# Performance work log

Measured on AMD Instinct MI355X. Metric: run time of the kernel, lower is better.

Reference implementation:

```python
import jax, jax.numpy as jnp
import numpy as np

N, F_IN, HID, HEADS, NCLS, E = 50000, 512, 64, 4, 64, 800000
NEG_SLOPE = 0.2
EPS = 1e-16


def setup_inputs() -> dict:
    key = jax.random.key(0)
    ks = jax.random.split(key, 10)
    s = 0.1
    return {
        "x": jax.random.normal(ks[0], (N, F_IN), jnp.float32),
        "edge_index": jax.random.randint(ks[1], (2, E), 0, N, jnp.int64),
        "W1": jax.random.normal(ks[2], (F_IN, HEADS * HID), jnp.float32) * s,
        "a_src1": jax.random.normal(ks[3], (HEADS, HID), jnp.float32) * s,
        "a_dst1": jax.random.normal(ks[4], (HEADS, HID), jnp.float32) * s,
        "b1": jax.random.normal(ks[5], (HEADS * HID,), jnp.float32) * s,
        "W2": jax.random.normal(ks[6], (HEADS * HID, NCLS), jnp.float32) * s,
        "a_src2": jax.random.normal(ks[7], (1, NCLS), jnp.float32) * s,
        "a_dst2": jax.random.normal(ks[8], (1, NCLS), jnp.float32) * s,
        "b2": jax.random.normal(ks[9], (NCLS,), jnp.float32) * s,
    }


def gat_conv(x, W, a_src, a_dst, b, src, dst):
    H, C = a_src.shape
    h = (x @ W).reshape(-1, H, C)                     # [N, H, C]
    # per-node attention halves, gathered per edge -> [E', H]
    al_src = jnp.einsum("nhc,hc->nh", h, a_src)
    al_dst = jnp.einsum("nhc,hc->nh", h, a_dst)
    e = jax.nn.leaky_relu(al_src[src] + al_dst[dst], NEG_SLOPE)
    # segment softmax over destination neighborhoods
    m = jax.ops.segment_max(e, dst, num_segments=x.shape[0])
    ex = jnp.exp(e - m[dst])
    denom = jax.ops.segment_sum(ex, dst, num_segments=x.shape[0])
    alpha = ex / (denom[dst] + EPS)                   # [E', H]
    out = jax.ops.segment_sum(alpha[:, :, None] * h[src], dst,
                              num_segments=x.shape[0])  # [N, H, C]
    return out.reshape(-1, H * C) + b


def reference(x, edge_index, W1, a_src1, a_dst1, b1, W2, a_src2, a_dst2, b2):
    n = x.shape[0]
    loop = jnp.arange(n, dtype=edge_index.dtype)
    src = jnp.concatenate([edge_index[0], loop])       # add self loops (PyG default)
    dst = jnp.concatenate([edge_index[1], loop])
    h = gat_conv(x, W1, a_src1, a_dst1, b1, src, dst)
    h = jax.nn.elu(h)                                  # dropout is identity in eval
    out = gat_conv(h, W2, a_src2, a_dst2, b2, src, dst)
    return jax.nn.log_softmax(out, axis=1)
```

## Files before the change

kernel.cpp:

```cpp
#include <hip/hip_runtime.h>
#include <math.h>

#define F_IN 512
#define HC1 256
#define HEADS 4
#define HID 64
#define NCLS 64
#define NEG_SLOPE 0.2f
#define EPS_DENOM 1e-16f

using short8 = __attribute__((ext_vector_type(8))) short;
using f32x4  = __attribute__((ext_vector_type(4))) float;

__device__ inline float wave_sum(float v) {
#pragma unroll
  for (int s = 32; s > 0; s >>= 1) v += __shfl_xor(v, s);
  return v;
}

__device__ inline unsigned short f2bf(float f) {
  unsigned int u = __float_as_uint(f);
  u = (u + 0x7FFF + ((u >> 16) & 1)) >> 16;
  return (unsigned short)u;
}
__device__ inline float bflo(unsigned int u) { return __uint_as_float(u << 16); }
__device__ inline float bfhi(unsigned int u) { return __uint_as_float(u & 0xFFFF0000u); }

__device__ inline unsigned int cvtpk_bf16(float lo, float hi) {
  unsigned int r;
  asm("v_cvt_pk_bf16_f32 %0, %1, %2" : "=v"(r) : "v"(lo), "v"(hi));
  return r;
}

__device__ inline void async_copy16(const void* g, void* l) {
  __builtin_amdgcn_global_load_lds((const __attribute__((address_space(1))) void*)g,
                                   (__attribute__((address_space(3))) void*)l, 16, 0, 0);
}

__global__ void castT_kernel(const float* __restrict__ W, unsigned short* __restrict__ WT,
                             int K, int Nn) {
  int id = blockIdx.x * blockDim.x + threadIdx.x;
  if (id >= K * Nn) return;
  int n = id / K, k = id % K;
  WT[id] = f2bf(W[(size_t)k * Nn + n]);
}


__global__ void hist_kernel(const int* __restrict__ dst, int E, int* __restrict__ cnt) {
  int i = blockIdx.x * blockDim.x + threadIdx.x;
  int stride = gridDim.x * blockDim.x;
  for (int e = i; e < E; e += stride) atomicAdd(&cnt[dst[e]], 1);
}

__global__ void scan_blocks_kernel(const int* __restrict__ cnt, int n,
                                   int* __restrict__ rowoff, int* __restrict__ cursor,
                                   int* __restrict__ bsum) {
  __shared__ int wpart[16];
  int b = blockIdx.x, tid = threadIdx.x;
  int i = b * 1024 + tid;
  int lane = tid & 63, wid = tid >> 6;
  int v = (i < n) ? (cnt[i] + 1) : 0;
  int x = v;
#pragma unroll
  for (int s = 1; s < 64; s <<= 1) {
    int t = __shfl_up(x, s);
    if (lane >= s) x += t;
  }
  if (lane == 63) wpart[wid] = x;
  __syncthreads();
  if (wid == 0) {
    int p = (lane < 16) ? wpart[lane] : 0;
#pragma unroll
    for (int s = 1; s < 16; s <<= 1) {
      int t = __shfl_up(p, s);
      if (lane >= s) p += t;
    }
    if (lane < 16) wpart[lane] = p;
  }
  __syncthreads();
  int incl = x + (wid ? wpart[wid - 1] : 0);
  if (i < n) { rowoff[i + 1] = incl; cursor[i] = incl - v; }
  if (tid == 1023) bsum[b] = incl;
  if (b == 0 && tid == 0) rowoff[0] = 0;
}

__global__ void scan_partials_kernel(int* __restrict__ bsum, int nb) {
  int lane = threadIdx.x;
  int v = (lane < nb) ? bsum[lane] : 0;
  int x = v;
#pragma unroll
  for (int s = 1; s < 64; s <<= 1) {
    int t = __shfl_up(x, s);
    if (lane >= s) x += t;
  }
  if (lane < nb) bsum[lane] = x - v;
}

__global__ void scan_add_kernel(int n, int* __restrict__ rowoff, int* __restrict__ cursor,
                                const int* __restrict__ bsum) {
  int i = blockIdx.x * 1024 + threadIdx.x;
  int off = bsum[blockIdx.x];
  if (i < n) { rowoff[i + 1] += off; cursor[i] += off; }
}

__global__ void scatter_kernel(const int* __restrict__ src, const int* __restrict__ dst,
                               int E, int n, int* __restrict__ cursor, int* __restrict__ esrc) {
  int i = blockIdx.x * blockDim.x + threadIdx.x;
  int stride = gridDim.x * blockDim.x;
  for (int e = i; e < E + n; e += stride) {
    int s, d;
    if (e < E) { s = src[e]; d = dst[e]; } else { s = e - E; d = s; }
    int pos = atomicAdd(&cursor[d], 1);
    esrc[pos] = s;
  }
}


__global__ __launch_bounds__(256)
void gemm1_fused_kernel(const float* __restrict__ A, const unsigned short* __restrict__ BT,
                        unsigned short* __restrict__ Cb,
                        const float* __restrict__ as1, const float* __restrict__ ad1,
                        float* __restrict__ als, float* __restrict__ ald, int M) {
  constexpr int BM = 64, BN = 256, BK = 32, K = F_IN, Nn = HC1;
  __shared__ float          Af[2][BM * BK];
  __shared__ unsigned short Bh[2][BN * BK];
  const int t = threadIdx.x;
  const int lane = t & 63;
  const int w = t >> 6;
  const int wc = w * 64;
  const int row0 = blockIdx.x * BM;
  const int lrow = lane & 15;
  const int lkf = (lane >> 4) * 8;

  auto stageA = [&](int buf, int k0) {
#pragma unroll
    for (int i = 0; i < 2; ++i) {
      int c = i * 256 + t;
      int r = c >> 3, slot = c & 7;
      int grow = row0 + r; if (grow > M - 1) grow = M - 1;
      const float* g = A + (size_t)grow * K + k0 + ((slot ^ (r & 7)) << 2);
      async_copy16(g, (char*)&Af[buf][0] + (size_t)(i * 256 + w * 64) * 16);
    }
  };
  auto stageB = [&](int buf, int k0) {
#pragma unroll
    for (int i = 0; i < 4; ++i) {
      int c = i * 256 + t;
      int r = c >> 2, slot = c & 3;
      const unsigned short* g = BT + (size_t)r * K + k0 + ((slot ^ (r & 3)) << 3);
      async_copy16(g, (char*)&Bh[buf][0] + (size_t)(i * 256 + w * 64) * 16);
    }
  };

  f32x4 acc[4][4] = {};
  stageA(0, 0); stageB(0, 0);
  int cur = 0;
  for (int k0 = 0; k0 < K; k0 += BK) {
    __syncthreads();
    if (k0 + BK < K) { stageA(cur ^ 1, k0 + BK); stageB(cur ^ 1, k0 + BK); }
    short8 a[4], b[4];
#pragma unroll
    for (int m = 0; m < 4; ++m) {
      int r = m * 16 + lrow;
      int s0 = lkf >> 2;
      const char* base = (const char*)&Af[cur][0] + (size_t)r * 128;
      float4 f0 = *(const float4*)(base + (((s0    ) ^ (r & 7)) << 4));
      float4 f1 = *(const float4*)(base + (((s0 | 1) ^ (r & 7)) << 4));
      union { short8 s; uint4 u; } pk;
      pk.u.x = cvtpk_bf16(f0.x, f0.y); pk.u.y = cvtpk_bf16(f0.z, f0.w);
      pk.u.z = cvtpk_bf16(f1.x, f1.y); pk.u.w = cvtpk_bf16(f1.z, f1.w);
      a[m] = pk.s;
    }
#pragma unroll
    for (int n = 0; n < 4; ++n) {
      int r = wc + n * 16 + lrow;
      int slot = lkf >> 3;
      b[n] = *(const short8*)((const char*)&Bh[cur][0] + (size_t)r * 64 +
                              (((slot ^ (r & 3))) << 4));
    }
#pragma unroll
    for (int m = 0; m < 4; ++m)
#pragma unroll
      for (int n = 0; n < 4; ++n)
        acc[m][n] = __builtin_amdgcn_mfma_f32_16x16x32_bf16(a[m], b[n], acc[m][n], 0, 0, 0);
    cur ^= 1;
  }

  float asv[4], adv[4];
#pragma unroll
  for (int n = 0; n < 4; ++n) {
    asv[n] = as1[w * 64 + n * 16 + lrow];
    adv[n] = ad1[w * 64 + n * 16 + lrow];
  }
#pragma unroll
  for (int m = 0; m < 4; ++m) {
#pragma unroll
    for (int j = 0; j < 4; ++j) {
      int r = row0 + m * 16 + (lane >> 4) * 4 + j;
      float ps = 0.f, pd = 0.f;
#pragma unroll
      for (int n = 0; n < 4; ++n) {
        float v = acc[m][n][j];
        ps += v * asv[n];
        pd += v * adv[n];
        if (r < M) Cb[(size_t)r * Nn + wc + n * 16 + lrow] = f2bf(v);
      }
#pragma unroll
      for (int s = 1; s < 16; s <<= 1) {
        ps += __shfl_xor(ps, s);
        pd += __shfl_xor(pd, s);
      }
      if ((lane & 15) == 0 && r < M) {
        als[r * HEADS + w] = ps;
        ald[r * HEADS + w] = pd;
      }
    }
  }
}


__global__ __launch_bounds__(256)
void gemm2_fused_kernel(const unsigned short* __restrict__ A,
                        const unsigned short* __restrict__ BT,
                        unsigned short* __restrict__ Cb,
                        const float* __restrict__ as2, const float* __restrict__ ad2,
                        float* __restrict__ als, float* __restrict__ ald, int M) {
  constexpr int BM = 128, BN = 64, BK = 32, K = HC1, Nn = NCLS;
  __shared__ unsigned short Alds[BM * BK];
  __shared__ unsigned short Blds[BN * BK];
  __shared__ float sps[BM], spd[BM];
  const int t = threadIdx.x;
  const int lane = t & 63;
  const int w = t >> 6;
  const int wr = (w >> 1) * 64;
  const int wc = (w & 1) * 32;
  const int row0 = blockIdx.x * BM;
  const int lrow = lane & 15;
  const int lk = (lane >> 4) * 8;
  if (t < BM) { sps[t] = 0.f; spd[t] = 0.f; }

  f32x4 acc[4][2] = {};
  for (int k0 = 0; k0 < K; k0 += BK) {
#pragma unroll
    for (int i = 0; i < 2; ++i) {
      int c = i * 256 + t;
      int arr = c >> 2;
      int ak = (c & 3) * 8;
      int grow = row0 + arr; if (grow > M - 1) grow = M - 1;
      const unsigned short* g = A + (size_t)grow * K + k0 + ak;
      unsigned short* l = Alds + (size_t)(i * 256 + w * 64) * 8;
      async_copy16(g, l);
    }
    {
      int c = t;
      int br = c >> 2;
      int bk = (c & 3) * 8;
      const unsigned short* g = BT + (size_t)br * K + k0 + bk;
      unsigned short* l = Blds + (size_t)(w * 64) * 8;
      async_copy16(g, l);
    }
    __syncthreads();
    short8 a[4], b[2];
#pragma unroll
    for (int m = 0; m < 4; ++m)
      a[m] = *(const short8*)&Alds[(wr + m * 16 + lrow) * BK + lk];
#pragma unroll
    for (int n = 0; n < 2; ++n)
      b[n] = *(const short8*)&Blds[(wc + n * 16 + lrow) * BK + lk];
#pragma unroll
    for (int m = 0; m < 4; ++m)
#pragma unroll
      for (int n = 0; n < 2; ++n)
        acc[m][n] = __builtin_amdgcn_mfma_f32_16x16x32_bf16(a[m], b[n], acc[m][n], 0, 0, 0);
    __syncthreads();
  }

  float asv[2], adv[2];
#pragma unroll
  for (int n = 0; n < 2; ++n) {
    asv[n] = as2[wc + n * 16 + lrow];
    adv[n] = ad2[wc + n * 16 + lrow];
  }
#pragma unroll
  for (int m = 0; m < 4; ++m) {
#pragma unroll
    for (int j = 0; j < 4; ++j) {
      int rl = wr + m * 16 + (lane >> 4) * 4 + j;
      int r = row0 + rl;
      float ps = 0.f, pd = 0.f;
#pragma unroll
      for (int n = 0; n < 2; ++n) {
        float v = acc[m][n][j];
        ps += v * asv[n];
        pd += v * adv[n];
        if (r < M) Cb[(size_t)r * Nn + wc + n * 16 + lrow] = f2bf(v);
      }
#pragma unroll
      for (int s = 1; s < 16; s <<= 1) {
        ps += __shfl_xor(ps, s);
        pd += __shfl_xor(pd, s);
      }
      if ((lane & 15) == 0) {
        atomicAdd(&sps[rl], ps);
        atomicAdd(&spd[rl], pd);
      }
    }
  }
  __syncthreads();
  if (t < BM) {
    int r = row0 + t;
    if (r < M) { als[r] = sps[t]; ald[r] = spd[t]; }
  }
}


__global__ void agg1_kernel(const unsigned short* __restrict__ h1b,
                            const float4* __restrict__ als1, const float4* __restrict__ ald1,
                            const int* __restrict__ rowoff, const int* __restrict__ esrc,
                            const float* __restrict__ b1, unsigned short* __restrict__ hact,
                            int n) {
  __shared__ float wlds[4][256];
  __shared__ int   slds[4][64];
  int w = threadIdx.x >> 6;
  int node = blockIdx.x * 4 + w;
  if (node >= n) return;
  int lane = threadIdx.x & 63;
  int hi = lane >> 5;
  int cl = lane & 31;
  int head = cl >> 3;
  int beg = rowoff[node], end = rowoff[node + 1];
  float4 aldn = ald1[node];
  f32x4 accA = {0.f, 0.f, 0.f, 0.f};
  f32x4 accB = {0.f, 0.f, 0.f, 0.f};
  float dl0 = 0.f, dl1 = 0.f, dl2 = 0.f, dl3 = 0.f;

  for (int base = beg; base < end; base += 64) {
    int cnt = min(64, end - base);
    if (lane < cnt) {
      int s = esrc[base + lane];
      float4 av = als1[s];
      float v, w0, w1, w2, w3;
      v = av.x + aldn.x; v = fmaxf(v, NEG_SLOPE * v); w0 = __expf(v);
      v = av.y + aldn.y; v = fmaxf(v, NEG_SLOPE * v); w1 = __expf(v);
      v = av.z + aldn.z; v = fmaxf(v, NEG_SLOPE * v); w2 = __expf(v);
      v = av.w + aldn.w; v = fmaxf(v, NEG_SLOPE * v); w3 = __expf(v);
      dl0 += w0; dl1 += w1; dl2 += w2; dl3 += w3;
      slds[w][lane] = s;
      float4 wv = {w0, w1, w2, w3};
      *(float4*)&wlds[w][lane * 4] = wv;
    }

    uint4 dA[4], dB[4];
    float wA[4], wB[4];
    auto ISSUE = [&](int j0, uint4* d, float* wj) {
#pragma unroll
      for (int ii = 0; ii < 4; ++ii) {
        int e = j0 + 2 * ii + hi;
        bool val = e < cnt;
        int se = val ? e : 0;
        int ss = slds[w][se];
        wj[ii] = val ? wlds[w][se * 4 + head] : 0.f;
        d[ii] = *(const uint4*)&h1b[(size_t)ss * HC1 + cl * 8];
      }
    };
    auto CONSUME = [&](const uint4* d, const float* wj) {
#pragma unroll
      for (int ii = 0; ii < 4; ++ii) {
        float q = wj[ii];
        accA[0] += q * bflo(d[ii].x); accA[1] += q * bfhi(d[ii].x);
        accA[2] += q * bflo(d[ii].y); accA[3] += q * bfhi(d[ii].y);
        accB[0] += q * bflo(d[ii].z); accB[1] += q * bfhi(d[ii].z);
        accB[2] += q * bflo(d[ii].w); accB[3] += q * bfhi(d[ii].w);
      }
    };

    ISSUE(0, dA, wA);
    for (int j0 = 8;; j0 += 16) {
      bool hasB = j0 < cnt;
      if (hasB) ISSUE(j0, dB, wB);
      CONSUME(dA, wA);
      if (!hasB) break;
      bool hasA = (j0 + 8) < cnt;
      if (hasA) ISSUE(j0 + 8, dA, wA);
      CONSUME(dB, wB);
      if (!hasA) break;
    }
  }

#pragma unroll
  for (int k = 0; k < 4; ++k) {
    accA[k] += __shfl_xor(accA[k], 32);
    accB[k] += __shfl_xor(accB[k], 32);
  }
  float d0 = wave_sum(dl0), d1 = wave_sum(dl1);
  float d2 = wave_sum(dl2), d3 = wave_sum(dl3);
  float den = head < 2 ? (head == 0 ? d0 : d1) : (head == 2 ? d2 : d3);
  float rden = 1.f / (den + EPS_DENOM);
  if (hi == 0) {
    float4 bv0 = *(const float4*)&b1[cl * 8];
    float4 bv1 = *(const float4*)&b1[cl * 8 + 4];
    float o[8];
    o[0] = accA[0] * rden + bv0.x; o[1] = accA[1] * rden + bv0.y;
    o[2] = accA[2] * rden + bv0.z; o[3] = accA[3] * rden + bv0.w;
    o[4] = accB[0] * rden + bv1.x; o[5] = accB[1] * rden + bv1.y;
    o[6] = accB[2] * rden + bv1.z; o[7] = accB[3] * rden + bv1.w;
    ushort4 ov0, ov1;
#pragma unroll
    for (int k = 0; k < 8; ++k) o[k] = o[k] > 0.f ? o[k] : __expf(o[k]) - 1.f;
    ov0.x = f2bf(o[0]); ov0.y = f2bf(o[1]); ov0.z = f2bf(o[2]); ov0.w = f2bf(o[3]);
    ov1.x = f2bf(o[4]); ov1.y = f2bf(o[5]); ov1.z = f2bf(o[6]); ov1.w = f2bf(o[7]);
    *(ushort4*)&hact[(size_t)node * HC1 + cl * 8] = ov0;
    *(ushort4*)&hact[(size_t)node * HC1 + cl * 8 + 4] = ov1;
  }
}

__global__ void agg2_kernel(const unsigned short* __restrict__ h2b,
                            const float* __restrict__ als2, const float* __restrict__ ald2,
                            const int* __restrict__ rowoff, const int* __restrict__ esrc,
                            const float* __restrict__ b2, float* __restrict__ out, int n) {
  __shared__ float wlds[4][64];
  __shared__ int   slds[4][64];
  int w = threadIdx.x >> 6;
  int node = blockIdx.x * 4 + w;
  if (node >= n) return;
  int lane = threadIdx.x & 63;
  int eg = lane >> 3;
  int cl = lane & 7;
  int beg = rowoff[node], end = rowoff[node + 1];
  float aldn = ald2[node];
  f32x4 accA = {0.f, 0.f, 0.f, 0.f};
  f32x4 accB = {0.f, 0.f, 0.f, 0.f};
  float dl = 0.f;
  for (int base = beg; base < end; base += 64) {
    int cnt = min(64, end - base);
    if (lane < cnt) {
      int s = esrc[base + lane];
      float v = als2[s] + aldn;
      v = fmaxf(v, NEG_SLOPE * v);
      float wl = __expf(v);
      dl += wl;
      slds[w][lane] = s;
      wlds[w][lane] = wl;
    }
    for (int j0 = 0; j0 < cnt; j0 += 32) {
      uint4 d[4]; float wj[4];
#pragma unroll
      for (int ii = 0; ii < 4; ++ii) {
        int e = j0 + ii * 8 + eg;
        bool val = e < cnt;
        int se = val ? e : 0;
        int ss = slds[w][se];
        wj[ii] = val ? wlds[w][se] : 0.f;
        d[ii] = *(const uint4*)&h2b[(size_t)ss * NCLS + cl * 8];
      }
#pragma unroll
      for (int ii = 0; ii < 4; ++ii) {
        float q = wj[ii];
        accA[0] += q * bflo(d[ii].x); accA[1] += q * bfhi(d[ii].x);
        accA[2] += q * bflo(d[ii].y); accA[3] += q * bfhi(d[ii].y);
        accB[0] += q * bflo(d[ii].z); accB[1] += q * bfhi(d[ii].z);
        accB[2] += q * bflo(d[ii].w); accB[3] += q * bfhi(d[ii].w);
      }
    }
  }
#pragma unroll
  for (int s = 8; s < 64; s <<= 1) {
#pragma unroll
    for (int k = 0; k < 4; ++k) {
      accA[k] += __shfl_xor(accA[k], s);
      accB[k] += __shfl_xor(accB[k], s);
    }
  }
  float den = wave_sum(dl);
  float rden = 1.f / (den + EPS_DENOM);
  float4 bv0 = *(const float4*)&b2[cl * 8];
  float4 bv1 = *(const float4*)&b2[cl * 8 + 4];
  float o[8];
  o[0] = accA[0] * rden + bv0.x; o[1] = accA[1] * rden + bv0.y;
  o[2] = accA[2] * rden + bv0.z; o[3] = accA[3] * rden + bv0.w;
  o[4] = accB[0] * rden + bv1.x; o[5] = accB[1] * rden + bv1.y;
  o[6] = accB[2] * rden + bv1.z; o[7] = accB[3] * rden + bv1.w;
  float mx = o[0];
#pragma unroll
  for (int k = 1; k < 8; ++k) mx = fmaxf(mx, o[k]);
#pragma unroll
  for (int s = 1; s < 8; s <<= 1) mx = fmaxf(mx, __shfl_xor(mx, s));
  float sm = 0.f;
#pragma unroll
  for (int k = 0; k < 8; ++k) sm += __expf(o[k] - mx);
#pragma unroll
  for (int s = 1; s < 8; s <<= 1) sm += __shfl_xor(sm, s);
  float ls = mx + __logf(sm);
  if (lane < 8) {
    float4 q0 = {o[0] - ls, o[1] - ls, o[2] - ls, o[3] - ls};
    float4 q1 = {o[4] - ls, o[5] - ls, o[6] - ls, o[7] - ls};
    *(float4*)&out[(size_t)node * NCLS + cl * 8] = q0;
    *(float4*)&out[(size_t)node * NCLS + cl * 8 + 4] = q1;
  }
}


extern "C" void kernel_launch(void* const* d_in, const int* in_sizes, int n_in,
                              void* d_out, int out_size, void* d_ws, size_t ws_size,
                              hipStream_t stream) {
  const float* x      = (const float*)d_in[0];
  const int*   eidx   = (const int*)d_in[1];
  const float* W1     = (const float*)d_in[2];
  const float* a_src1 = (const float*)d_in[3];
  const float* a_dst1 = (const float*)d_in[4];
  const float* b1     = (const float*)d_in[5];
  const float* W2     = (const float*)d_in[6];
  const float* a_src2 = (const float*)d_in[7];
  const float* a_dst2 = (const float*)d_in[8];
  const float* b2     = (const float*)d_in[9];
  float* out = (float*)d_out;

  const int Nn = in_sizes[0] / F_IN;
  const int E  = in_sizes[1] / 2;
  const int* esrc_in = eidx;
  const int* edst_in = eidx + E;

  char* ws = (char*)d_ws;
  size_t off = 0;
  auto alloc = [&](size_t bytes) -> void* {
    void* p = ws + off;
    off += (bytes + 255) & ~(size_t)255;
    return p;
  };
  unsigned short* h1b    = (unsigned short*)alloc((size_t)Nn * HC1 * sizeof(short));
  unsigned short* hact   = (unsigned short*)alloc((size_t)Nn * HC1 * sizeof(short));
  unsigned short* h2b    = (unsigned short*)alloc((size_t)Nn * NCLS * sizeof(short));
  unsigned short* W1T    = (unsigned short*)alloc((size_t)F_IN * HC1 * sizeof(short));
  unsigned short* W2T    = (unsigned short*)alloc((size_t)HC1 * NCLS * sizeof(short));
  float*          als1   = (float*)alloc((size_t)Nn * HEADS * sizeof(float));
  float*          ald1   = (float*)alloc((size_t)Nn * HEADS * sizeof(float));
  float*          als2   = (float*)alloc((size_t)Nn * sizeof(float));
  float*          ald2   = (float*)alloc((size_t)Nn * sizeof(float));
  int*            cnt    = (int*)alloc((size_t)Nn * sizeof(int));
  int*            rowoff = (int*)alloc((size_t)(Nn + 1) * sizeof(int));
  int*            cursor = (int*)alloc((size_t)Nn * sizeof(int));
  int*            bsum   = (int*)alloc(256 * sizeof(int));
  int*            esrc   = (int*)alloc((size_t)(E + Nn) * sizeof(int));

  const int nscan = (Nn + 1023) / 1024;

  castT_kernel<<<(F_IN * HC1 + 255) / 256, 256, 0, stream>>>(W1, W1T, F_IN, HC1);
  castT_kernel<<<(HC1 * NCLS + 255) / 256, 256, 0, stream>>>(W2, W2T, HC1, NCLS);

  hipMemsetAsync(cnt, 0, (size_t)Nn * sizeof(int), stream);
  hist_kernel<<<(E + 255) / 256, 256, 0, stream>>>(edst_in, E, cnt);
  scan_blocks_kernel<<<nscan, 1024, 0, stream>>>(cnt, Nn, rowoff, cursor, bsum);
  scan_partials_kernel<<<1, 64, 0, stream>>>(bsum, nscan);
  scan_add_kernel<<<nscan, 1024, 0, stream>>>(Nn, rowoff, cursor, bsum);
  scatter_kernel<<<(E + Nn + 255) / 256, 256, 0, stream>>>(esrc_in, edst_in, E, Nn, cursor, esrc);

  {
    int blocks = (Nn + 63) / 64;
    gemm1_fused_kernel<<<blocks, 256, 0, stream>>>(x, W1T, h1b, a_src1, a_dst1,
                                                   als1, ald1, Nn);
    int ablocks = (Nn + 3) / 4;
    agg1_kernel<<<ablocks, 256, 0, stream>>>(h1b, (const float4*)als1, (const float4*)ald1,
                                             rowoff, esrc, b1, hact, Nn);
  }

  {
    int blocks = (Nn + 127) / 128;
    gemm2_fused_kernel<<<blocks, 256, 0, stream>>>(hact, W2T, h2b, a_src2, a_dst2,
                                                   als2, ald2, Nn);
    int ablocks = (Nn + 3) / 4;
    agg2_kernel<<<ablocks, 256, 0, stream>>>(h2b, als2, ald2, rowoff, esrc, b2, out, Nn);
  }
}
```

Measured before the change: 266.5 us.

## Replace LDS-staged GEMMs with direct global-to-register MFMA operand loads

```diff
diff --git a/kernel.cpp b/kernel.cpp
--- a/kernel.cpp
+++ b/kernel.cpp
@@ -30,11 +30,6 @@
   unsigned int r;
   asm("v_cvt_pk_bf16_f32 %0, %1, %2" : "=v"(r) : "v"(lo), "v"(hi));
   return r;
-}
-
-__device__ inline void async_copy16(const void* g, void* l) {
-  __builtin_amdgcn_global_load_lds((const __attribute__((address_space(1))) void*)g,
-                                   (__attribute__((address_space(3))) void*)l, 16, 0, 0);
 }
 
 __global__ void castT_kernel(const float* __restrict__ W, unsigned short* __restrict__ WT,
@@ -117,73 +112,51 @@
 
 
 __global__ __launch_bounds__(256)
-void gemm1_fused_kernel(const float* __restrict__ A, const unsigned short* __restrict__ BT,
-                        unsigned short* __restrict__ Cb,
-                        const float* __restrict__ as1, const float* __restrict__ ad1,
-                        float* __restrict__ als, float* __restrict__ ald, int M) {
-  constexpr int BM = 64, BN = 256, BK = 32, K = F_IN, Nn = HC1;
-  __shared__ float          Af[2][BM * BK];
-  __shared__ unsigned short Bh[2][BN * BK];
+void gemm1_reg_kernel(const float* __restrict__ A, const unsigned short* __restrict__ BT,
+                      unsigned short* __restrict__ Cb,
+                      const float* __restrict__ as1, const float* __restrict__ ad1,
+                      float* __restrict__ als, float* __restrict__ ald, int M) {
+  constexpr int K = F_IN, Nn = HC1;
   const int t = threadIdx.x;
   const int lane = t & 63;
   const int w = t >> 6;
   const int wc = w * 64;
-  const int row0 = blockIdx.x * BM;
+  const int row0 = blockIdx.x * 64;
   const int lrow = lane & 15;
-  const int lkf = (lane >> 4) * 8;
-
-  auto stageA = [&](int buf, int k0) {
-#pragma unroll
-    for (int i = 0; i < 2; ++i) {
-      int c = i * 256 + t;
-      int r = c >> 3, slot = c & 7;
-      int grow = row0 + r; if (grow > M - 1) grow = M - 1;
-      const float* g = A + (size_t)grow * K + k0 + ((slot ^ (r & 7)) << 2);
-      async_copy16(g, (char*)&Af[buf][0] + (size_t)(i * 256 + w * 64) * 16);
-    }
-  };
-  auto stageB = [&](int buf, int k0) {
-#pragma unroll
-    for (int i = 0; i < 4; ++i) {
-      int c = i * 256 + t;
-      int r = c >> 2, slot = c & 3;
-      const unsigned short* g = BT + (size_t)r * K + k0 + ((slot ^ (r & 3)) << 3);
-      async_copy16(g, (char*)&Bh[buf][0] + (size_t)(i * 256 + w * 64) * 16);
-    }
-  };
+  const int lk = (lane >> 4) * 8;
+
+  const float* ap[4];
+#pragma unroll
+  for (int m = 0; m < 4; ++m) {
+    int r = row0 + m * 16 + lrow; if (r > M - 1) r = M - 1;
+    ap[m] = A + (size_t)r * K + lk;
+  }
+  const unsigned short* bp[4];
+#pragma unroll
+  for (int n = 0; n < 4; ++n)
+    bp[n] = BT + (size_t)(wc + n * 16 + lrow) * K + lk;
 
   f32x4 acc[4][4] = {};
-  stageA(0, 0); stageB(0, 0);
-  int cur = 0;
-  for (int k0 = 0; k0 < K; k0 += BK) {
-    __syncthreads();
-    if (k0 + BK < K) { stageA(cur ^ 1, k0 + BK); stageB(cur ^ 1, k0 + BK); }
+#pragma unroll 2
+  for (int k0 = 0; k0 < K; k0 += 32) {
     short8 a[4], b[4];
 #pragma unroll
     for (int m = 0; m < 4; ++m) {
-      int r = m * 16 + lrow;
-      int s0 = lkf >> 2;
-      const char* base = (const char*)&Af[cur][0] + (size_t)r * 128;
-      float4 f0 = *(const float4*)(base + (((s0    ) ^ (r & 7)) << 4));
-      float4 f1 = *(const float4*)(base + (((s0 | 1) ^ (r & 7)) << 4));
+      float4 f0 = *(const float4*)(ap[m] + k0);
+      float4 f1 = *(const float4*)(ap[m] + k0 + 4);
       union { short8 s; uint4 u; } pk;
       pk.u.x = cvtpk_bf16(f0.x, f0.y); pk.u.y = cvtpk_bf16(f0.z, f0.w);
       pk.u.z = cvtpk_bf16(f1.x, f1.y); pk.u.w = cvtpk_bf16(f1.z, f1.w);
       a[m] = pk.s;
     }
 #pragma unroll
-    for (int n = 0; n < 4; ++n) {
-      int r = wc + n * 16 + lrow;
-      int slot = lkf >> 3;
-      b[n] = *(const short8*)((const char*)&Bh[cur][0] + (size_t)r * 64 +
-                              (((slot ^ (r & 3))) << 4));
-    }
+    for (int n = 0; n < 4; ++n)
+      b[n] = *(const short8*)(bp[n] + k0);
 #pragma unroll
     for (int m = 0; m < 4; ++m)
 #pragma unroll
       for (int n = 0; n < 4; ++n)
         acc[m][n] = __builtin_amdgcn_mfma_f32_16x16x32_bf16(a[m], b[n], acc[m][n], 0, 0, 0);
-    cur ^= 1;
   }
 
   float asv[4], adv[4];
@@ -220,96 +193,74 @@
 
 
 __global__ __launch_bounds__(256)
-void gemm2_fused_kernel(const unsigned short* __restrict__ A,
-                        const unsigned short* __restrict__ BT,
-                        unsigned short* __restrict__ Cb,
-                        const float* __restrict__ as2, const float* __restrict__ ad2,
-                        float* __restrict__ als, float* __restrict__ ald, int M) {
-  constexpr int BM = 128, BN = 64, BK = 32, K = HC1, Nn = NCLS;
-  __shared__ unsigned short Alds[BM * BK];
-  __shared__ unsigned short Blds[BN * BK];
-  __shared__ float sps[BM], spd[BM];
+void gemm2_reg_kernel(const unsigned short* __restrict__ A,
+                      const unsigned short* __restrict__ BT,
+                      unsigned short* __restrict__ Cb,
+                      const float* __restrict__ as2, const float* __restrict__ ad2,
+                      float* __restrict__ als, float* __restrict__ ald, int M) {
+  constexpr int K = HC1, Nn = NCLS;
   const int t = threadIdx.x;
   const int lane = t & 63;
   const int w = t >> 6;
-  const int wr = (w >> 1) * 64;
-  const int wc = (w & 1) * 32;
-  const int row0 = blockIdx.x * BM;
+  const int row0 = blockIdx.x * 256 + w * 64;
   const int lrow = lane & 15;
   const int lk = (lane >> 4) * 8;
-  if (t < BM) { sps[t] = 0.f; spd[t] = 0.f; }
-
-  f32x4 acc[4][2] = {};
-  for (int k0 = 0; k0 < K; k0 += BK) {
-#pragma unroll
-    for (int i = 0; i < 2; ++i) {
-      int c = i * 256 + t;
-      int arr = c >> 2;
-      int ak = (c & 3) * 8;
-      int grow = row0 + arr; if (grow > M - 1) grow = M - 1;
-      const unsigned short* g = A + (size_t)grow * K + k0 + ak;
-      unsigned short* l = Alds + (size_t)(i * 256 + w * 64) * 8;
-      async_copy16(g, l);
-    }
-    {
-      int c = t;
-      int br = c >> 2;
-      int bk = (c & 3) * 8;
-      const unsigned short* g = BT + (size_t)br * K + k0 + bk;
-      unsigned short* l = Blds + (size_t)(w * 64) * 8;
-      async_copy16(g, l);
-    }
-    __syncthreads();
-    short8 a[4], b[2];
+
+  const unsigned short* ap[4];
+#pragma unroll
+  for (int m = 0; m < 4; ++m) {
+    int r = row0 + m * 16 + lrow; if (r > M - 1) r = M - 1;
+    ap[m] = A + (size_t)r * K + lk;
+  }
+  const unsigned short* bp[4];
+#pragma unroll
+  for (int n = 0; n < 4; ++n)
+    bp[n] = BT + (size_t)(n * 16 + lrow) * K + lk;
+
+  f32x4 acc[4][4] = {};
+#pragma unroll 2
+  for (int k0 = 0; k0 < K; k0 += 32) {
+    short8 a[4], b[4];
+#pragma unroll
+    for (int m = 0; m < 4; ++m) a[m] = *(const short8*)(ap[m] + k0);
+#pragma unroll
+    for (int n = 0; n < 4; ++n) b[n] = *(const short8*)(bp[n] + k0);
 #pragma unroll
     for (int m = 0; m < 4; ++m)
-      a[m] = *(const short8*)&Alds[(wr + m * 16 + lrow) * BK + lk];
-#pragma unroll
-    for (int n = 0; n < 2; ++n)
-      b[n] = *(const short8*)&Blds[(wc + n * 16 + lrow) * BK + lk];
-#pragma unroll
-    for (int m = 0; m < 4; ++m)
-#pragma unroll
-      for (int n = 0; n < 2; ++n)
+#pragma unroll
+      for (int n = 0; n < 4; ++n)
         acc[m][n] = __builtin_amdgcn_mfma_f32_16x16x32_bf16(a[m], b[n], acc[m][n], 0, 0, 0);
-    __syncthreads();
-  }
-
-  float asv[2], adv[2];
-#pragma unroll
-  for (int n = 0; n < 2; ++n) {
-    asv[n] = as2[wc + n * 16 + lrow];
-    adv[n] = ad2[wc + n * 16 + lrow];
+  }
+
+  float asv[4], adv[4];
+#pragma unroll
+  for (int n = 0; n < 4; ++n) {
+    asv[n] = as2[n * 16 + lrow];
+    adv[n] = ad2[n * 16 + lrow];
   }
 #pragma unroll
   for (int m = 0; m < 4; ++m) {
 #pragma unroll
     for (int j = 0; j < 4; ++j) {
-      int rl = wr + m * 16 + (lane >> 4) * 4 + j;
-      int r = row0 + rl;
+      int r = row0 + m * 16 + (lane >> 4) * 4 + j;
       float ps = 0.f, pd = 0.f;
 #pragma unroll
-      for (int n = 0; n < 2; ++n) {
+      for (int n = 0; n < 4; ++n) {
         float v = acc[m][n][j];
         ps += v * asv[n];
         pd += v * adv[n];
-        if (r < M) Cb[(size_t)r * Nn + wc + n * 16 + lrow] = f2bf(v);
+        if (r < M) Cb[(size_t)r * Nn + n * 16 + lrow] = f2bf(v);
       }
 #pragma unroll
       for (int s = 1; s < 16; s <<= 1) {
         ps += __shfl_xor(ps, s);
         pd += __shfl_xor(pd, s);
       }
-      if ((lane & 15) == 0) {
-        atomicAdd(&sps[rl], ps);
-        atomicAdd(&spd[rl], pd);
-      }
-    }
-  }
-  __syncthreads();
-  if (t < BM) {
-    int r = row0 + t;
-    if (r < M) { als[r] = sps[t]; ald[r] = spd[t]; }
+      if ((lane & 15) == 0 && r < M) {
+        als[r] = ps;
+        ald[r] = pd;
+      }
+    }
   }
 }
 
@@ -556,17 +507,17 @@
 
   {
     int blocks = (Nn + 63) / 64;
-    gemm1_fused_kernel<<<blocks, 256, 0, stream>>>(x, W1T, h1b, a_src1, a_dst1,
-                                                   als1, ald1, Nn);
+    gemm1_reg_kernel<<<blocks, 256, 0, stream>>>(x, W1T, h1b, a_src1, a_dst1,
+                                                 als1, ald1, Nn);
     int ablocks = (Nn + 3) / 4;
     agg1_kernel<<<ablocks, 256, 0, stream>>>(h1b, (const float4*)als1, (const float4*)ald1,
                                              rowoff, esrc, b1, hact, Nn);
   }
 
   {
-    int blocks = (Nn + 127) / 128;
-    gemm2_fused_kernel<<<blocks, 256, 0, stream>>>(hact, W2T, h2b, a_src2, a_dst2,
-                                                   als2, ald2, Nn);
+    int blocks = (Nn + 255) / 256;
+    gemm2_reg_kernel<<<blocks, 256, 0, stream>>>(hact, W2T, h2b, a_src2, a_dst2,
+                                                 als2, ald2, Nn);
     int ablocks = (Nn + 3) / 4;
     agg2_kernel<<<ablocks, 256, 0, stream>>>(h2b, als2, ald2, rowoff, esrc, b2, out, Nn);
   }
```

After: 325.7 us. 22.2% more time.
